# Performance work log

Measured on AMD Instinct MI355X. Metric: run time of the kernel, lower is better.

## Reference

```python
import jax, jax.numpy as jnp
from jax import lax
import numpy as np

# branch input selection (0 = real, 1 = imag) for the 8 T_att branches A..H
Q_IDX = np.array([0, 0, 1, 1, 0, 0, 1, 1])
K_IDX = np.array([0, 1, 0, 1, 0, 1, 0, 1])
V_IDX = np.array([0, 1, 1, 0, 1, 0, 0, 1])

H_DIM = 16  # LSTM hidden / out_channel


def _ln(x, w, b, eps=1e-5):
    m = x.mean(-1, keepdims=True)
    v = x.var(-1, keepdims=True)  # biased var, matches torch LayerNorm
    return (x - m) / jnp.sqrt(v + eps) * w + b


def _lstm(x, Wih, Whh, bih, bhh):
    # x: [B, T, C]; Wih: [4H, C]; Whh: [4H, H]; gate order i, f, g, o (torch)
    B = x.shape[0]
    H = Whh.shape[1]
    xg = jnp.einsum('btc,gc->btg', x, Wih) + bih + bhh  # [B, T, 4H]

    def step(carry, xg_t):
        h, c = carry
        g = xg_t + h @ Whh.T
        i, f, gg, o = jnp.split(g, 4, axis=-1)
        c = jax.nn.sigmoid(f) * c + jax.nn.sigmoid(i) * jnp.tanh(gg)
        h = jax.nn.sigmoid(o) * jnp.tanh(c)
        return (h, c), h

    h0 = jnp.zeros((B, H), x.dtype)
    _, hs = lax.scan(step, (h0, h0), jnp.swapaxes(xg, 0, 1))
    return jnp.swapaxes(hs, 0, 1)  # [B, T, H]


def _t_att(q, k, v, Wih, Whh, bih, bhh):
    # Wih: [3, 4H, C] for (query, key, value) LSTMs
    query = _lstm(q, Wih[0], Whh[0], bih[0], bhh[0])
    key = _lstm(k, Wih[1], Whh[1], bih[1], bhh[1])
    value = _lstm(v, Wih[2], Whh[2], bih[2], bhh[2])
    T = q.shape[1]
    energy = jnp.einsum('btf,bsf->bts', query, key) / 4.0  # / sqrt(16)
    mask = jnp.tril(jnp.ones((T, T), q.dtype))  # multiplicative causal mask
    energy = jax.nn.softmax(energy * mask, axis=-1)
    return jnp.einsum('bts,bsf->btf', energy, value)


def _forward(inputs, Wih, Whh, bih, bhh, ln1_w, ln1_b, ln2_w, ln2_b,
             lin_r_w, lin_r_b, lin_i_w, lin_i_b, ln3_w, ln3_b, prelu_a):
    N, C, F, T, ri = inputs.shape
    x = inputs.transpose(0, 2, 3, 1, 4).reshape(N * F, T, C, ri)  # [B, T, C, 2]
    # layernorm1 over C (applied per real/imag)
    x = jnp.swapaxes(_ln(jnp.swapaxes(x, 2, 3), ln1_w, ln1_b), 2, 3)
    real, imag = x[..., 0], x[..., 1]
    ri_stack = jnp.stack([real, imag])  # [2, B, T, C]
    q_in, k_in, v_in = ri_stack[Q_IDX], ri_stack[K_IDX], ri_stack[V_IDX]  # [8, B, T, C]
    att = jax.vmap(_t_att)(q_in, k_in, v_in, Wih, Whh, bih, bhh)  # [8, B, T, 16]
    real_att = att[0] - att[1] - att[2] - att[3]
    imag_att = att[4] + att[5] + att[6] - att[7]
    y = jnp.stack([real_att, imag_att], -1)  # [B, T, 16, 2]
    # layernorm2 over out_channel=16
    y = jnp.swapaxes(_ln(jnp.swapaxes(y, 2, 3), ln2_w, ln2_b), 2, 3)
    x_real, x_imag = y[..., 0], y[..., 1]  # [B, T, 16]
    pr = lambda z: z @ lin_r_w.T + lin_r_b
    pi = lambda z: z @ lin_i_w.T + lin_i_b
    out_real = pr(x_real) - pi(x_imag)  # [B, T, C]
    out_imag = pr(x_imag) + pi(x_real)
    out_real = out_real.reshape(N, F, T, C).transpose(0, 3, 1, 2)  # [N, C, F, T]
    out_imag = out_imag.reshape(N, F, T, C).transpose(0, 3, 1, 2)
    outs = jnp.stack([out_real, out_imag], -1)  # [N, C, F, T, 2]
    # layernorm3 over C
    outs = jnp.swapaxes(_ln(jnp.swapaxes(outs, 1, 4), ln3_w, ln3_b), 1, 4)
    outs = jnp.where(outs >= 0, outs, prelu_a * outs)  # PReLU (scalar a)
    # dropout is identity in eval mode
    return outs + inputs


def setup_inputs() -> dict:
    key = jax.random.key(0)
    ks = jax.random.split(key, 12)
    N, C, F, T = 4, 64, 100, 200
    H = H_DIM
    bound = 1.0 / np.sqrt(H)  # torch LSTM/Linear(16->64) init bound = 0.25
    u = lambda k, shape: jax.random.uniform(k, shape, jnp.float32, -bound, bound)
    return {
        'inputs': jax.random.normal(ks[0], (N, C, F, T, 2), jnp.float32),
        'Wih': u(ks[1], (8, 3, 4 * H, C)),
        'Whh': u(ks[2], (8, 3, 4 * H, H)),
        'bih': u(ks[3], (8, 3, 4 * H)),
        'bhh': u(ks[4], (8, 3, 4 * H)),
        'ln1_w': jnp.ones((C,), jnp.float32), 'ln1_b': jnp.zeros((C,), jnp.float32),
        'ln2_w': jnp.ones((H,), jnp.float32), 'ln2_b': jnp.zeros((H,), jnp.float32),
        'lin_r_w': u(ks[5], (C, H)), 'lin_r_b': u(ks[6], (C,)),
        'lin_i_w': u(ks[7], (C, H)), 'lin_i_b': u(ks[8], (C,)),
        'ln3_w': jnp.ones((C,), jnp.float32), 'ln3_b': jnp.zeros((C,), jnp.float32),
        'prelu_a': jnp.array(0.25, jnp.float32),
    }


def reference(inputs, Wih, Whh, bih, bhh, ln1_w, ln1_b, ln2_w, ln2_b,
              lin_r_w, lin_r_b, lin_i_w, lin_i_b, ln3_w, ln3_b, prelu_a):
    return _forward(inputs, Wih, Whh, bih, bhh, ln1_w, ln1_b, ln2_w, ln2_b,
                    lin_r_w, lin_r_b, lin_i_w, lin_i_b, ln3_w, ln3_b, prelu_a)
```

## Files before the change

### kernel.cpp

```cpp
#include <hip/hip_runtime.h>
#include <hip/hip_bf16.h>


typedef __attribute__((ext_vector_type(8))) short bf16x8;
typedef __attribute__((ext_vector_type(4))) float f32x4;
typedef __attribute__((ext_vector_type(2))) float f32x2;

static __device__ __forceinline__ float bf2f(unsigned short u) {
  return __uint_as_float(((unsigned)u) << 16);
}
static __device__ __forceinline__ unsigned short f2bfu(float x) {
  __hip_bfloat16 h = __float2bfloat16(x);
  return *(unsigned short*)&h;
}
static __device__ __forceinline__ float sigf(float x) {
  return __fdividef(1.f, 1.f + __expf(-x));
}
static __device__ __forceinline__ float tanh_(float x) {
  return 1.f - __fdividef(2.f, __expf(2.f * x) + 1.f);
}
static __device__ __forceinline__ f32x2 hh2(float v) {
  f32x2 r; r.x = v; r.y = v; return r;
}

template <int CTRL>
static __device__ __forceinline__ float dpp_bcast(float x) {
  int xi = __float_as_int(x);
  int r = __builtin_amdgcn_update_dpp(xi, xi, CTRL, 0xF, 0xF, false);
  return __int_as_float(r);
}

__global__ __launch_bounds__(256) void k_ln1(const float* __restrict__ in,
    const float* __restrict__ w, const float* __restrict__ bsh,
    unsigned short* __restrict__ xr, unsigned short* __restrict__ xi, int b0) {
  __shared__ float is[64][101];
  __shared__ float os[100][65];
  int bid = blockIdx.x;
  int nfl = bid >> 2, tile = bid & 3;
  int nf = b0 + nfl;
  int t0 = tile * 50;
  int n = nf / 100, f = nf - n * 100;
  int tid = threadIdx.x;
  for (int i = 0; i < 7; ++i) {
    int idx = tid + i * 256;
    if (idx < 1600) {
      int c = idx / 25, q = idx - c * 25;
      float4 v = *(const float4*)(in + (size_t)((n * 64 + c) * 100 + f) * 400
                                  + t0 * 2 + q * 4);
      is[c][q*4+0] = v.x; is[c][q*4+1] = v.y; is[c][q*4+2] = v.z; is[c][q*4+3] = v.w;
    }
  }
  __syncthreads();
  if (tid < 100) {
    float s = 0.f, ss = 0.f;
    #pragma unroll
    for (int c = 0; c < 64; ++c) { float v = is[c][tid]; s += v; ss += v * v; }
    float mean = s * 0.015625f;
    float var  = ss * 0.015625f - mean * mean;
    float rstd = rsqrtf(var + 1e-5f);
    #pragma unroll
    for (int c = 0; c < 64; ++c)
      os[tid][c] = (is[c][tid] - mean) * rstd * w[c] + bsh[c];
  }
  __syncthreads();
  for (int ri = 0; ri < 2; ++ri) {
    unsigned short* dst = ri ? xi : xr;
    for (int i = 0; i < 4; ++i) {
      int idx = tid + i * 256;
      if (idx < 800) {
        int t = idx >> 4, q = idx & 15;
        ushort4 v;
        v.x = f2bfu(os[t*2+ri][q*4+0]); v.y = f2bfu(os[t*2+ri][q*4+1]);
        v.z = f2bfu(os[t*2+ri][q*4+2]); v.w = f2bfu(os[t*2+ri][q*4+3]);
        *(ushort4*)(dst + ((size_t)nfl * 200 + t0 + t) * 64 + q * 4) = v;
      }
    }
  }
}

__global__ void k_prep(const float* __restrict__ bih, const float* __restrict__ bhh,
                       const float* __restrict__ Wih, float* __restrict__ bihh,
                       unsigned short* __restrict__ wbf) {
  int i = blockIdx.x * 256 + threadIdx.x;
  if (i < 1536) bihh[i] = bih[i] + bhh[i];
  if (i < 98304) wbf[i] = f2bfu(Wih[i]);
}

__global__ __launch_bounds__(64) void k_lstm(const unsigned short* __restrict__ xr,
    const unsigned short* __restrict__ xi, const unsigned short* __restrict__ wbf,
    const float* __restrict__ bihh, const float* __restrict__ Whh,
    float* __restrict__ hbuf, int NB, int nbq) {
  __shared__ f32x2 wl[2][16][17];
  int lane = threadIdx.x;
  int q = lane >> 4, c = lane & 15;
  int lq = blockIdx.x / nbq, q4 = blockIdx.x - lq * nbq;
  int l = lq;
  int b = q4 * 4 + q; if (b >= NB) b = NB - 1;
  const float* Wg = Whh + (size_t)l * 1024;
  for (int idx = lane; idx < 1024; idx += 64) {
    int row = idx >> 4, col = idx & 15;
    int gate = row >> 4, kk = row & 15;
    ((float*)&wl[gate >> 1][kk][col])[gate & 1] = Wg[idx];
  }
  __syncthreads();
  const f32x2* wla = wl[0][c];
  const f32x2* wlb = wl[1][c];
  int sel = (0xE54770 >> l) & 1;
  const unsigned short* xs = sel ? xi : xr;
  int ba = q4 * 4 + (c >> 2); if (ba >= NB) ba = NB - 1;
  const unsigned short* ap2 = xs + ((size_t)ba * 200 + (c & 3)) * 64 + q * 8;
  const unsigned short* wrow = wbf + l * 4096 + c * 64 + q * 8;
  float bv0 = bihh[l * 64 + c], bv1 = bihh[l * 64 + 16 + c];
  float bv2 = bihh[l * 64 + 32 + c], bv3 = bihh[l * 64 + 48 + c];
  f32x4 zb0 = {bv0, bv0, bv0, bv0}, zb1 = {bv1, bv1, bv1, bv1};
  f32x4 zb2 = {bv2, bv2, bv2, bv2}, zb3 = {bv3, bv3, bv3, bv3};
  float* hp = hbuf + ((size_t)l * NB + b) * 3200 + c;
  float h = 0.f, cs = 0.f;
  int tcur = 0;
#define MG1(DST, OFS, ZB, A0v, A1v) { \
  bf16x8 w0_ = *(const bf16x8*)(wrow + OFS); \
  bf16x8 w1_ = *(const bf16x8*)(wrow + OFS + 32); \
  f32x4 t_ = __builtin_amdgcn_mfma_f32_16x16x32_bf16(A0v, w0_, ZB, 0, 0, 0); \
  DST = __builtin_amdgcn_mfma_f32_16x16x32_bf16(A1v, w1_, t_, 0, 0, 0); }
#define MGROUP(D0, D1, D2, D3, A0v, A1v) \
  MG1(D0, 0, zb0, A0v, A1v) MG1(D1, 1024, zb1, A0v, A1v) \
  MG1(D2, 2048, zb2, A0v, A1v) MG1(D3, 3072, zb3, A0v, A1v)
#define HV(i) dpp_bcast<0x150 + i>(h)
#define LSTEP2(AC0, AC1, AC2, AC3, FLD) { \
  float hv0  = HV(0),  hv1  = HV(1),  hv2  = HV(2),  hv3  = HV(3);  \
  float hv4  = HV(4),  hv5  = HV(5),  hv6  = HV(6),  hv7  = HV(7);  \
  float hv8  = HV(8),  hv9  = HV(9),  hv10 = HV(10), hv11 = HV(11); \
  float hv12 = HV(12), hv13 = HV(13), hv14 = HV(14), hv15 = HV(15); \
  f32x2 pA = {AC0.FLD, AC1.FLD}; \
  f32x2 qA = {AC2.FLD, AC3.FLD}; \
  f32x2 pB = {0.f, 0.f}, qB = {0.f, 0.f}; \
  pA += wla[0]  * hh2(hv0);  pB += wla[1]  * hh2(hv1);  \
  qA += wlb[0]  * hh2(hv0);  qB += wlb[1]  * hh2(hv1);  \
  pA += wla[2]  * hh2(hv2);  pB += wla[3]  * hh2(hv3);  \
  qA += wlb[2]  * hh2(hv2);  qB += wlb[3]  * hh2(hv3);  \
  pA += wla[4]  * hh2(hv4);  pB += wla[5]  * hh2(hv5);  \
  qA += wlb[4]  * hh2(hv4);  qB += wlb[5]  * hh2(hv5);  \
  pA += wla[6]  * hh2(hv6);  pB += wla[7]  * hh2(hv7);  \
  qA += wlb[6]  * hh2(hv6);  qB += wlb[7]  * hh2(hv7);  \
  pA += wla[8]  * hh2(hv8);  pB += wla[9]  * hh2(hv9);  \
  qA += wlb[8]  * hh2(hv8);  qB += wlb[9]  * hh2(hv9);  \
  pA += wla[10] * hh2(hv10); pB += wla[11] * hh2(hv11); \
  qA += wlb[10] * hh2(hv10); qB += wlb[11] * hh2(hv11); \
  pA += wla[12] * hh2(hv12); pB += wla[13] * hh2(hv13); \
  qA += wlb[12] * hh2(hv12); qB += wlb[13] * hh2(hv13); \
  pA += wla[14] * hh2(hv14); pB += wla[15] * hh2(hv15); \
  qA += wlb[14] * hh2(hv14); qB += wlb[15] * hh2(hv15); \
  f32x2 p01 = pA + pB, p23 = qA + qB; \
  float ig_ = sigf(p01.x), fg_ = sigf(p01.y); \
  float gg_ = tanh_(p23.x), og_ = sigf(p23.y); \
  cs = fg_ * cs + ig_ * gg_; \
  h = og_ * tanh_(cs); \
  hp[tcur * 16] = h; ++tcur; }
  bf16x8 a0 = *(const bf16x8*)(ap2), a1 = *(const bf16x8*)(ap2 + 32);
  f32x4 c0, c1, c2, c3, n0, n1, n2, n3;
  MGROUP(c0, c1, c2, c3, a0, a1);
  ap2 += 256;
  a0 = *(const bf16x8*)(ap2); a1 = *(const bf16x8*)(ap2 + 32);
  for (int g = 0; g < 50; ++g) {
    LSTEP2(c0, c1, c2, c3, x)
    LSTEP2(c0, c1, c2, c3, y)
    MGROUP(n0, n1, n2, n3, a0, a1);
    if (g < 48) ap2 += 256;
    a0 = *(const bf16x8*)(ap2); a1 = *(const bf16x8*)(ap2 + 32);
    LSTEP2(c0, c1, c2, c3, z)
    LSTEP2(c0, c1, c2, c3, w)
    c0 = n0; c1 = n1; c2 = n2; c3 = n3;
  }
#undef LSTEP2
#undef HV
#undef MGROUP
#undef MG1
}

__global__ __launch_bounds__(256) void k_attn(const float* __restrict__ hbuf,
                                              float* __restrict__ att, int NB) {
  __shared__ float Q[200][17];
  __shared__ float K[200][16];
  __shared__ float V[200][16];
  __shared__ float Vs[200][17];
  int bid = blockIdx.x;
  int br = bid / NB, b = bid - br * NB;
  int tid = threadIdx.x;
  const float* qg = hbuf + ((size_t)(br * 3 + 0) * NB + b) * 3200;
  const float* kg = hbuf + ((size_t)(br * 3 + 1) * NB + b) * 3200;
  const float* vg = hbuf + ((size_t)(br * 3 + 2) * NB + b) * 3200;
  for (int i = 0; i < 4; ++i) {
    int idx = tid + i * 256;
    if (idx < 800) {
      int t = idx >> 2, q = idx & 3;
      float4 a = *(const float4*)(qg + t * 16 + q * 4);
      Q[t][q*4+0] = a.x; Q[t][q*4+1] = a.y; Q[t][q*4+2] = a.z; Q[t][q*4+3] = a.w;
      *(float4*)&K[t][q * 4] = *(const float4*)(kg + t * 16 + q * 4);
      *(float4*)&V[t][q * 4] = *(const float4*)(vg + t * 16 + q * 4);
    }
  }
  __syncthreads();
  if (tid < 16) {
    float acc = 0.f;
    Vs[199][tid] = 0.f;
    for (int t = 198; t >= 0; --t) { acc += V[t + 1][tid]; Vs[t][tid] = acc; }
  }
  __syncthreads();
  if (tid < 200) {
    int t = tid;
    float q0[16], va[16];
    #pragma unroll
    for (int k = 0; k < 16; ++k) q0[k] = Q[t][k] * 0.25f;
    #pragma unroll
    for (int k = 0; k < 16; ++k) va[k] = Vs[t][k];
    float S = (float)(199 - t);
    for (int s = 0; s <= t; ++s) {
      float e = 0.f;
      #pragma unroll
      for (int k = 0; k < 16; ++k) e += q0[k] * K[s][k];
      float wgt = __expf(e);
      S += wgt;
      #pragma unroll
      for (int k = 0; k < 16; ++k) va[k] += wgt * V[s][k];
    }
    float inv = __fdividef(1.f, S);
    float* dst = att + (((size_t)br * NB + b) * 200 + t) * 16;
    #pragma unroll
    for (int q = 0; q < 4; ++q) {
      float4 v; v.x = va[q*4+0]*inv; v.y = va[q*4+1]*inv;
      v.z = va[q*4+2]*inv; v.w = va[q*4+3]*inv;
      *(float4*)(dst + q * 4) = v;
    }
  }
}

__global__ __launch_bounds__(256) void k_out(const float* __restrict__ att,
    const float* __restrict__ in,
    const float* __restrict__ ln2w, const float* __restrict__ ln2b,
    const float* __restrict__ lrw, const float* __restrict__ lrb,
    const float* __restrict__ liw, const float* __restrict__ lib,
    const float* __restrict__ ln3w, const float* __restrict__ ln3b,
    const float* __restrict__ pa, float* __restrict__ out, int b0, int NB) {
  __shared__ float as_[8][40][17];
  __shared__ float ys[40][2][17];
  __shared__ float zs[64][81];
  int bid = blockIdx.x;
  int nfl = bid / 5, tile = bid - nfl * 5;
  int nf = b0 + nfl;
  int t0 = tile * 40;
  int n = nf / 100, f = nf - n * 100;
  int tid = threadIdx.x;
  for (int i = 0; i < 5; ++i) {
    int idx = tid + i * 256;
    int br = idx / 160, r = idx - br * 160;
    int t = r >> 2, q = r & 3;
    float4 v = *(const float4*)(att + (((size_t)br * NB + nfl) * 200 + t0 + t) * 16 + q * 4);
    as_[br][t][q*4+0] = v.x; as_[br][t][q*4+1] = v.y;
    as_[br][t][q*4+2] = v.z; as_[br][t][q*4+3] = v.w;
  }
  __syncthreads();
  if (tid < 80) {
    int t = tid >> 1, ri = tid & 1;
    float vv[16]; float s = 0.f, ss = 0.f;
    #pragma unroll
    for (int k = 0; k < 16; ++k) {
      float v;
      if (ri == 0) v = as_[0][t][k] - as_[1][t][k] - as_[2][t][k] - as_[3][t][k];
      else         v = as_[4][t][k] + as_[5][t][k] + as_[6][t][k] - as_[7][t][k];
      vv[k] = v; s += v; ss += v * v;
    }
    float mean = s * 0.0625f;
    float var  = ss * 0.0625f - mean * mean;
    float rstd = rsqrtf(var + 1e-5f);
    #pragma unroll
    for (int k = 0; k < 16; ++k)
      ys[t][ri][k] = (vv[k] - mean) * rstd * ln2w[k] + ln2b[k];
  }
  __syncthreads();
  int wv = tid >> 6, cc = tid & 63;
  float lr[16], li[16];
  #pragma unroll
  for (int q = 0; q < 4; ++q) {
    float4 v = *(const float4*)(lrw + cc * 16 + q * 4);
    lr[q*4+0] = v.x; lr[q*4+1] = v.y; lr[q*4+2] = v.z; lr[q*4+3] = v.w;
    float4 u = *(const float4*)(liw + cc * 16 + q * 4);
    li[q*4+0] = u.x; li[q*4+1] = u.y; li[q*4+2] = u.z; li[q*4+3] = u.w;
  }
  float brc = lrb[cc], bic = lib[cc];
  float w3 = ln3w[cc], b3 = ln3b[cc];
  float aP = pa[0];
  for (int tt = wv; tt < 40; tt += 4) {
    float zr = brc - bic, zi = brc + bic;
    #pragma unroll
    for (int k = 0; k < 16; ++k) {
      float yr = ys[tt][0][k], yi = ys[tt][1][k];
      zr += yr * lr[k] - yi * li[k];
      zi += yi * lr[k] + yr * li[k];
    }
    float s1 = zr, s2 = zr * zr, s3 = zi, s4 = zi * zi;
    #pragma unroll
    for (int m = 1; m < 64; m <<= 1) {
      s1 += __shfl_xor(s1, m, 64);
      s2 += __shfl_xor(s2, m, 64);
      s3 += __shfl_xor(s3, m, 64);
      s4 += __shfl_xor(s4, m, 64);
    }
    float mr = s1 * 0.015625f, vr = s2 * 0.015625f - mr * mr;
    float mi = s3 * 0.015625f, vi = s4 * 0.015625f - mi * mi;
    float r1 = (zr - mr) * rsqrtf(vr + 1e-5f) * w3 + b3;
    float r2 = (zi - mi) * rsqrtf(vi + 1e-5f) * w3 + b3;
    r1 = r1 >= 0.f ? r1 : aP * r1;
    r2 = r2 >= 0.f ? r2 : aP * r2;
    zs[cc][tt * 2 + 0] = r1;
    zs[cc][tt * 2 + 1] = r2;
  }
  __syncthreads();
  for (int i = 0; i < 5; ++i) {
    int idx = tid + i * 256;
    int c = idx / 20, q = idx - c * 20;
    size_t gaddr = (size_t)((n * 64 + c) * 100 + f) * 400 + t0 * 2 + q * 4;
    float4 v = *(const float4*)(in + gaddr);
    float4 z;
    z.x = zs[c][q*4+0] + v.x; z.y = zs[c][q*4+1] + v.y;
    z.z = zs[c][q*4+2] + v.z; z.w = zs[c][q*4+3] + v.w;
    *(float4*)(out + gaddr) = z;
  }
}

extern "C" void kernel_launch(void* const* d_in, const int* in_sizes, int n_in,
                              void* d_out, int out_size, void* d_ws, size_t ws_size,
                              hipStream_t stream) {
  (void)in_sizes; (void)n_in; (void)out_size;
  const float* inputs = (const float*)d_in[0];
  const float* Wih  = (const float*)d_in[1];
  const float* Whh  = (const float*)d_in[2];
  const float* bih  = (const float*)d_in[3];
  const float* bhh  = (const float*)d_in[4];
  const float* ln1w = (const float*)d_in[5];
  const float* ln1b = (const float*)d_in[6];
  const float* ln2w = (const float*)d_in[7];
  const float* ln2b = (const float*)d_in[8];
  const float* lrw  = (const float*)d_in[9];
  const float* lrb  = (const float*)d_in[10];
  const float* liw  = (const float*)d_in[11];
  const float* lib  = (const float*)d_in[12];
  const float* ln3w = (const float*)d_in[13];
  const float* ln3b = (const float*)d_in[14];
  const float* pa   = (const float*)d_in[15];
  float* out = (float*)d_out;
  char* ws = (char*)d_ws;

  int NB = 400;
  while (NB > 25 && 204800ull + (size_t)NB * 460800ull > ws_size) NB /= 2;
  int nch = 400 / NB;

  float* bihh = (float*)(ws + 0);
  unsigned short* wbf = (unsigned short*)(ws + 8192);
  size_t o_xr = 204800;
  size_t o_xi = o_xr + (size_t)NB * 25600;
  size_t o_h  = o_xi + (size_t)NB * 25600;
  size_t o_at = o_h  + (size_t)NB * 307200;
  unsigned short* xr = (unsigned short*)(ws + o_xr);
  unsigned short* xi = (unsigned short*)(ws + o_xi);
  float* hbuf = (float*)(ws + o_h);
  float* att  = (float*)(ws + o_at);

  k_prep<<<384, 256, 0, stream>>>(bih, bhh, Wih, bihh, wbf);
  int nbq = (NB + 3) >> 2;
  for (int ch = 0; ch < nch; ++ch) {
    int b0 = ch * NB;
    k_ln1 <<<NB * 4,   256, 0, stream>>>(inputs, ln1w, ln1b, xr, xi, b0);
    k_lstm<<<24 * nbq,  64, 0, stream>>>(xr, xi, wbf, bihh, Whh, hbuf, NB, nbq);
    k_attn<<<8 * NB,   256, 0, stream>>>(hbuf, att, NB);
    k_out <<<NB * 5,   256, 0, stream>>>(att, inputs, ln2w, ln2b, lrw, lrb,
                                         liw, lib, ln3w, ln3b, pa, out, b0, NB);
  }
}
```

Measured before the change: 507.8 us.

## Interleave two independent LSTM batch groups per wavefront to hide recurrence latency

Each k_lstm block now processes two groups of four sequences, interleaving their recurrent steps so the serial dpp/FMA/transcendental dependency chain of one group overlaps with the other. This halves the number of blocks and amortizes the shared-memory Whh load across more work. It raises register pressure and reduces grid size, which could lower occupancy or leave CUs idle if the block count falls below the CU count.

```diff
diff --git a/kernel.cpp b/kernel.cpp
--- a/kernel.cpp
+++ b/kernel.cpp
@@ -89,13 +89,14 @@
 __global__ __launch_bounds__(64) void k_lstm(const unsigned short* __restrict__ xr,
     const unsigned short* __restrict__ xi, const unsigned short* __restrict__ wbf,
     const float* __restrict__ bihh, const float* __restrict__ Whh,
-    float* __restrict__ hbuf, int NB, int nbq) {
+    float* __restrict__ hbuf, int NB, int nbq, int npair) {
   __shared__ f32x2 wl[2][16][17];
   int lane = threadIdx.x;
   int q = lane >> 4, c = lane & 15;
-  int lq = blockIdx.x / nbq, q4 = blockIdx.x - lq * nbq;
+  int lq = blockIdx.x / npair, pr = blockIdx.x - lq * npair;
   int l = lq;
-  int b = q4 * 4 + q; if (b >= NB) b = NB - 1;
+  int g0 = pr * 2;
+  int g1 = g0 + 1; if (g1 >= nbq) g1 = g0;
   const float* Wg = Whh + (size_t)l * 1024;
   for (int idx = lane; idx < 1024; idx += 64) {
     int row = idx >> 4, col = idx & 15;
@@ -107,16 +108,20 @@
   const f32x2* wlb = wl[1][c];
   int sel = (0xE54770 >> l) & 1;
   const unsigned short* xs = sel ? xi : xr;
-  int ba = q4 * 4 + (c >> 2); if (ba >= NB) ba = NB - 1;
-  const unsigned short* ap2 = xs + ((size_t)ba * 200 + (c & 3)) * 64 + q * 8;
+  int bA = g0 * 4 + q; if (bA >= NB) bA = NB - 1;
+  int bB = g1 * 4 + q; if (bB >= NB) bB = NB - 1;
+  int baA = g0 * 4 + (c >> 2); if (baA >= NB) baA = NB - 1;
+  int baB = g1 * 4 + (c >> 2); if (baB >= NB) baB = NB - 1;
+  const unsigned short* apA = xs + ((size_t)baA * 200 + (c & 3)) * 64 + q * 8;
+  const unsigned short* apB = xs + ((size_t)baB * 200 + (c & 3)) * 64 + q * 8;
   const unsigned short* wrow = wbf + l * 4096 + c * 64 + q * 8;
   float bv0 = bihh[l * 64 + c], bv1 = bihh[l * 64 + 16 + c];
   float bv2 = bihh[l * 64 + 32 + c], bv3 = bihh[l * 64 + 48 + c];
   f32x4 zb0 = {bv0, bv0, bv0, bv0}, zb1 = {bv1, bv1, bv1, bv1};
   f32x4 zb2 = {bv2, bv2, bv2, bv2}, zb3 = {bv3, bv3, bv3, bv3};
-  float* hp = hbuf + ((size_t)l * NB + b) * 3200 + c;
-  float h = 0.f, cs = 0.f;
-  int tcur = 0;
+  float* hpA = hbuf + ((size_t)l * NB + bA) * 3200 + c;
+  float* hpB = hbuf + ((size_t)l * NB + bB) * 3200 + c;
+  float hA = 0.f, csA = 0.f, hB = 0.f, csB = 0.f;
 #define MG1(DST, OFS, ZB, A0v, A1v) { \
   bf16x8 w0_ = *(const bf16x8*)(wrow + OFS); \
   bf16x8 w1_ = *(const bf16x8*)(wrow + OFS + 32); \
@@ -125,54 +130,66 @@
 #define MGROUP(D0, D1, D2, D3, A0v, A1v) \
   MG1(D0, 0, zb0, A0v, A1v) MG1(D1, 1024, zb1, A0v, A1v) \
   MG1(D2, 2048, zb2, A0v, A1v) MG1(D3, 3072, zb3, A0v, A1v)
-#define HV(i) dpp_bcast<0x150 + i>(h)
-#define LSTEP2(AC0, AC1, AC2, AC3, FLD) { \
-  float hv0  = HV(0),  hv1  = HV(1),  hv2  = HV(2),  hv3  = HV(3);  \
-  float hv4  = HV(4),  hv5  = HV(5),  hv6  = HV(6),  hv7  = HV(7);  \
-  float hv8  = HV(8),  hv9  = HV(9),  hv10 = HV(10), hv11 = HV(11); \
-  float hv12 = HV(12), hv13 = HV(13), hv14 = HV(14), hv15 = HV(15); \
-  f32x2 pA = {AC0.FLD, AC1.FLD}; \
-  f32x2 qA = {AC2.FLD, AC3.FLD}; \
-  f32x2 pB = {0.f, 0.f}, qB = {0.f, 0.f}; \
-  pA += wla[0]  * hh2(hv0);  pB += wla[1]  * hh2(hv1);  \
-  qA += wlb[0]  * hh2(hv0);  qB += wlb[1]  * hh2(hv1);  \
-  pA += wla[2]  * hh2(hv2);  pB += wla[3]  * hh2(hv3);  \
-  qA += wlb[2]  * hh2(hv2);  qB += wlb[3]  * hh2(hv3);  \
-  pA += wla[4]  * hh2(hv4);  pB += wla[5]  * hh2(hv5);  \
-  qA += wlb[4]  * hh2(hv4);  qB += wlb[5]  * hh2(hv5);  \
-  pA += wla[6]  * hh2(hv6);  pB += wla[7]  * hh2(hv7);  \
-  qA += wlb[6]  * hh2(hv6);  qB += wlb[7]  * hh2(hv7);  \
-  pA += wla[8]  * hh2(hv8);  pB += wla[9]  * hh2(hv9);  \
-  qA += wlb[8]  * hh2(hv8);  qB += wlb[9]  * hh2(hv9);  \
-  pA += wla[10] * hh2(hv10); pB += wla[11] * hh2(hv11); \
-  qA += wlb[10] * hh2(hv10); qB += wlb[11] * hh2(hv11); \
-  pA += wla[12] * hh2(hv12); pB += wla[13] * hh2(hv13); \
-  qA += wlb[12] * hh2(hv12); qB += wlb[13] * hh2(hv13); \
-  pA += wla[14] * hh2(hv14); pB += wla[15] * hh2(hv15); \
-  qA += wlb[14] * hh2(hv14); qB += wlb[15] * hh2(hv15); \
-  f32x2 p01 = pA + pB, p23 = qA + qB; \
+#define HVX(i, H) dpp_bcast<0x150 + i>(H)
+#define LSTEP2(H, CS, HP, AC0, AC1, AC2, AC3, FLD, TT) { \
+  float hv0  = HVX(0,H),  hv1  = HVX(1,H),  hv2  = HVX(2,H),  hv3  = HVX(3,H);  \
+  float hv4  = HVX(4,H),  hv5  = HVX(5,H),  hv6  = HVX(6,H),  hv7  = HVX(7,H);  \
+  float hv8  = HVX(8,H),  hv9  = HVX(9,H),  hv10 = HVX(10,H), hv11 = HVX(11,H); \
+  float hv12 = HVX(12,H), hv13 = HVX(13,H), hv14 = HVX(14,H), hv15 = HVX(15,H); \
+  f32x2 pA_ = {AC0.FLD, AC1.FLD}; \
+  f32x2 qA_ = {AC2.FLD, AC3.FLD}; \
+  f32x2 pB_ = {0.f, 0.f}, qB_ = {0.f, 0.f}; \
+  pA_ += wla[0]  * hh2(hv0);  pB_ += wla[1]  * hh2(hv1);  \
+  qA_ += wlb[0]  * hh2(hv0);  qB_ += wlb[1]  * hh2(hv1);  \
+  pA_ += wla[2]  * hh2(hv2);  pB_ += wla[3]  * hh2(hv3);  \
+  qA_ += wlb[2]  * hh2(hv2);  qB_ += wlb[3]  * hh2(hv3);  \
+  pA_ += wla[4]  * hh2(hv4);  pB_ += wla[5]  * hh2(hv5);  \
+  qA_ += wlb[4]  * hh2(hv4);  qB_ += wlb[5]  * hh2(hv5);  \
+  pA_ += wla[6]  * hh2(hv6);  pB_ += wla[7]  * hh2(hv7);  \
+  qA_ += wlb[6]  * hh2(hv6);  qB_ += wlb[7]  * hh2(hv7);  \
+  pA_ += wla[8]  * hh2(hv8);  pB_ += wla[9]  * hh2(hv9);  \
+  qA_ += wlb[8]  * hh2(hv8);  qB_ += wlb[9]  * hh2(hv9);  \
+  pA_ += wla[10] * hh2(hv10); pB_ += wla[11] * hh2(hv11); \
+  qA_ += wlb[10] * hh2(hv10); qB_ += wlb[11] * hh2(hv11); \
+  pA_ += wla[12] * hh2(hv12); pB_ += wla[13] * hh2(hv13); \
+  qA_ += wlb[12] * hh2(hv12); qB_ += wlb[13] * hh2(hv13); \
+  pA_ += wla[14] * hh2(hv14); pB_ += wla[15] * hh2(hv15); \
+  qA_ += wlb[14] * hh2(hv14); qB_ += wlb[15] * hh2(hv15); \
+  f32x2 p01 = pA_ + pB_, p23 = qA_ + qB_; \
   float ig_ = sigf(p01.x), fg_ = sigf(p01.y); \
   float gg_ = tanh_(p23.x), og_ = sigf(p23.y); \
-  cs = fg_ * cs + ig_ * gg_; \
-  h = og_ * tanh_(cs); \
-  hp[tcur * 16] = h; ++tcur; }
-  bf16x8 a0 = *(const bf16x8*)(ap2), a1 = *(const bf16x8*)(ap2 + 32);
-  f32x4 c0, c1, c2, c3, n0, n1, n2, n3;
-  MGROUP(c0, c1, c2, c3, a0, a1);
-  ap2 += 256;
-  a0 = *(const bf16x8*)(ap2); a1 = *(const bf16x8*)(ap2 + 32);
+  CS = fg_ * CS + ig_ * gg_; \
+  H = og_ * tanh_(CS); \
+  HP[(TT) * 16] = H; }
+  bf16x8 aA0 = *(const bf16x8*)(apA), aA1 = *(const bf16x8*)(apA + 32);
+  bf16x8 aB0 = *(const bf16x8*)(apB), aB1 = *(const bf16x8*)(apB + 32);
+  f32x4 cA0, cA1, cA2, cA3, nA0, nA1, nA2, nA3;
+  f32x4 cB0, cB1, cB2, cB3, nB0, nB1, nB2, nB3;
+  MGROUP(cA0, cA1, cA2, cA3, aA0, aA1);
+  MGROUP(cB0, cB1, cB2, cB3, aB0, aB1);
+  apA += 256; apB += 256;
+  aA0 = *(const bf16x8*)(apA); aA1 = *(const bf16x8*)(apA + 32);
+  aB0 = *(const bf16x8*)(apB); aB1 = *(const bf16x8*)(apB + 32);
   for (int g = 0; g < 50; ++g) {
-    LSTEP2(c0, c1, c2, c3, x)
-    LSTEP2(c0, c1, c2, c3, y)
-    MGROUP(n0, n1, n2, n3, a0, a1);
-    if (g < 48) ap2 += 256;
-    a0 = *(const bf16x8*)(ap2); a1 = *(const bf16x8*)(ap2 + 32);
-    LSTEP2(c0, c1, c2, c3, z)
-    LSTEP2(c0, c1, c2, c3, w)
-    c0 = n0; c1 = n1; c2 = n2; c3 = n3;
+    int t4 = g * 4;
+    LSTEP2(hA, csA, hpA, cA0, cA1, cA2, cA3, x, t4)
+    LSTEP2(hB, csB, hpB, cB0, cB1, cB2, cB3, x, t4)
+    LSTEP2(hA, csA, hpA, cA0, cA1, cA2, cA3, y, t4 + 1)
+    LSTEP2(hB, csB, hpB, cB0, cB1, cB2, cB3, y, t4 + 1)
+    MGROUP(nA0, nA1, nA2, nA3, aA0, aA1);
+    MGROUP(nB0, nB1, nB2, nB3, aB0, aB1);
+    if (g < 48) { apA += 256; apB += 256; }
+    aA0 = *(const bf16x8*)(apA); aA1 = *(const bf16x8*)(apA + 32);
+    aB0 = *(const bf16x8*)(apB); aB1 = *(const bf16x8*)(apB + 32);
+    LSTEP2(hA, csA, hpA, cA0, cA1, cA2, cA3, z, t4 + 2)
+    LSTEP2(hB, csB, hpB, cB0, cB1, cB2, cB3, z, t4 + 2)
+    LSTEP2(hA, csA, hpA, cA0, cA1, cA2, cA3, w, t4 + 3)
+    LSTEP2(hB, csB, hpB, cB0, cB1, cB2, cB3, w, t4 + 3)
+    cA0 = nA0; cA1 = nA1; cA2 = nA2; cA3 = nA3;
+    cB0 = nB0; cB1 = nB1; cB2 = nB2; cB3 = nB3;
   }
 #undef LSTEP2
-#undef HV
+#undef HVX
 #undef MGROUP
 #undef MG1
 }
@@ -367,12 +384,14 @@
 
   k_prep<<<384, 256, 0, stream>>>(bih, bhh, Wih, bihh, wbf);
   int nbq = (NB + 3) >> 2;
+  int npair = (nbq + 1) >> 1;
   for (int ch = 0; ch < nch; ++ch) {
     int b0 = ch * NB;
-    k_ln1 <<<NB * 4,   256, 0, stream>>>(inputs, ln1w, ln1b, xr, xi, b0);
-    k_lstm<<<24 * nbq,  64, 0, stream>>>(xr, xi, wbf, bihh, Whh, hbuf, NB, nbq);
-    k_attn<<<8 * NB,   256, 0, stream>>>(hbuf, att, NB);
-    k_out <<<NB * 5,   256, 0, stream>>>(att, inputs, ln2w, ln2b, lrw, lrb,
-                                         liw, lib, ln3w, ln3b, pa, out, b0, NB);
-  }
-}
+    k_ln1 <<<NB * 4,     256, 0, stream>>>(inputs, ln1w, ln1b, xr, xi, b0);
+    k_lstm<<<24 * npair,  64, 0, stream>>>(xr, xi, wbf, bihh, Whh, hbuf,
+                                           NB, nbq, npair);
+    k_attn<<<8 * NB,     256, 0, stream>>>(hbuf, att, NB);
+    k_out <<<NB * 5,     256, 0, stream>>>(att, inputs, ln2w, ln2b, lrw, lrb,
+                                           liw, lib, ln3w, ln3b, pa, out, b0, NB);
+  }
+}
```

Result: slower. 566.5 us (+11.6%).

## Compute causal attention with bf16 MFMA tiles for QK and PV

Applied to the files above, without the earlier changes.

Replaces the scalar per-row attention loop with wave-level 16x16x32 bf16 MFMA tiles. Each wave computes QK scores, exponentiates them with the multiplicative-mask semantics (masked keys get weight 1), and stages P in LDS to feed a second MFMA against V stored transposed. Row sums are reduced with shuffles. The intent is to cut the serial per-thread dot-product cost. In exchange, Q, K, V and P are rounded to bf16, and the kernel reads padded rows past t=199.

```diff
diff --git a/kernel.cpp b/kernel.cpp
--- a/kernel.cpp
+++ b/kernel.cpp
@@ -179,58 +179,91 @@
 
 __global__ __launch_bounds__(256) void k_attn(const float* __restrict__ hbuf,
                                               float* __restrict__ att, int NB) {
-  __shared__ float Q[200][17];
-  __shared__ float K[200][16];
-  __shared__ float V[200][16];
-  __shared__ float Vs[200][17];
+  __shared__ unsigned short Kb[224][40];
+  __shared__ unsigned short Vt[16][232];
+  __shared__ unsigned short Pc[4][16][40];
   int bid = blockIdx.x;
   int br = bid / NB, b = bid - br * NB;
   int tid = threadIdx.x;
   const float* qg = hbuf + ((size_t)(br * 3 + 0) * NB + b) * 3200;
   const float* kg = hbuf + ((size_t)(br * 3 + 1) * NB + b) * 3200;
   const float* vg = hbuf + ((size_t)(br * 3 + 2) * NB + b) * 3200;
+  {
+    unsigned* kz = (unsigned*)&Kb[0][0];
+    for (int i = tid; i < 4480; i += 256) kz[i] = 0;
+    unsigned* vz = (unsigned*)&Vt[0][0];
+    for (int i = tid; i < 1856; i += 256) vz[i] = 0;
+  }
+  __syncthreads();
   for (int i = 0; i < 4; ++i) {
     int idx = tid + i * 256;
     if (idx < 800) {
-      int t = idx >> 2, q = idx & 3;
-      float4 a = *(const float4*)(qg + t * 16 + q * 4);
-      Q[t][q*4+0] = a.x; Q[t][q*4+1] = a.y; Q[t][q*4+2] = a.z; Q[t][q*4+3] = a.w;
-      *(float4*)&K[t][q * 4] = *(const float4*)(kg + t * 16 + q * 4);
-      *(float4*)&V[t][q * 4] = *(const float4*)(vg + t * 16 + q * 4);
-    }
-  }
-  __syncthreads();
-  if (tid < 16) {
-    float acc = 0.f;
-    Vs[199][tid] = 0.f;
-    for (int t = 198; t >= 0; --t) { acc += V[t + 1][tid]; Vs[t][tid] = acc; }
-  }
-  __syncthreads();
-  if (tid < 200) {
-    int t = tid;
-    float q0[16], va[16];
-    #pragma unroll
-    for (int k = 0; k < 16; ++k) q0[k] = Q[t][k] * 0.25f;
-    #pragma unroll
-    for (int k = 0; k < 16; ++k) va[k] = Vs[t][k];
-    float S = (float)(199 - t);
-    for (int s = 0; s <= t; ++s) {
-      float e = 0.f;
+      int s = idx >> 2, qq = idx & 3;
+      float4 kv = *(const float4*)(kg + s * 16 + qq * 4);
+      ushort4 kp;
+      kp.x = f2bfu(kv.x); kp.y = f2bfu(kv.y);
+      kp.z = f2bfu(kv.z); kp.w = f2bfu(kv.w);
+      *(ushort4*)&Kb[s][qq * 4] = kp;
+      float4 vv = *(const float4*)(vg + s * 16 + qq * 4);
+      Vt[qq * 4 + 0][s] = f2bfu(vv.x);
+      Vt[qq * 4 + 1][s] = f2bfu(vv.y);
+      Vt[qq * 4 + 2][s] = f2bfu(vv.z);
+      Vt[qq * 4 + 3][s] = f2bfu(vv.w);
+    }
+  }
+  __syncthreads();
+  int w = tid >> 6, lane = tid & 63;
+  int q = lane >> 4, n = lane & 15;
+  size_t obase = (size_t)(br * NB + b) * 200;
+  for (int m = w; m <= 12; m += 4) {
+    bf16x8 aQ;
+    {
+      int trow = 16 * m + n;
+      const float* qp = qg + trow * 16 + q * 8;
       #pragma unroll
-      for (int k = 0; k < 16; ++k) e += q0[k] * K[s][k];
-      float wgt = __expf(e);
-      S += wgt;
+      for (int e = 0; e < 8; ++e) {
+        float v = (q < 2) ? qp[e] * 0.25f : 0.f;
+        aQ[e] = (short)f2bfu(v);
+      }
+    }
+    f32x4 pv = {0.f, 0.f, 0.f, 0.f};
+    float s40 = 0.f, s41 = 0.f, s42 = 0.f, s43 = 0.f;
+    #pragma unroll 1
+    for (int jj = 0; jj < 7; ++jj) {
+      int sb = jj * 32;
+      bf16x8 bK0 = *(const bf16x8*)&Kb[sb + n][q * 8];
+      bf16x8 bK1 = *(const bf16x8*)&Kb[sb + 16 + n][q * 8];
+      f32x4 z = {0.f, 0.f, 0.f, 0.f};
+      f32x4 d0 = __builtin_amdgcn_mfma_f32_16x16x32_bf16(aQ, bK0, z, 0, 0, 0);
+      f32x4 d1 = __builtin_amdgcn_mfma_f32_16x16x32_bf16(aQ, bK1, z, 0, 0, 0);
+      int s0 = sb + n, s1 = sb + 16 + n;
+      int tb = 16 * m + 4 * q;
       #pragma unroll
-      for (int k = 0; k < 16; ++k) va[k] += wgt * V[s][k];
-    }
-    float inv = __fdividef(1.f, S);
-    float* dst = att + (((size_t)br * NB + b) * 200 + t) * 16;
-    #pragma unroll
-    for (int q = 0; q < 4; ++q) {
-      float4 v; v.x = va[q*4+0]*inv; v.y = va[q*4+1]*inv;
-      v.z = va[q*4+2]*inv; v.w = va[q*4+3]*inv;
-      *(float4*)(dst + q * 4) = v;
-    }
+      for (int r = 0; r < 4; ++r) {
+        int t = tb + r;
+        float p0 = (s0 > 199) ? 0.f : ((s0 > t) ? 1.f : __expf(d0[r]));
+        float p1 = (s1 > 199) ? 0.f : ((s1 > t) ? 1.f : __expf(d1[r]));
+        if (r == 0) { s40 += p0 + p1; } else if (r == 1) { s41 += p0 + p1; }
+        else if (r == 2) { s42 += p0 + p1; } else { s43 += p0 + p1; }
+        Pc[w][4 * q + r][n]      = f2bfu(p0);
+        Pc[w][4 * q + r][16 + n] = f2bfu(p1);
+      }
+      bf16x8 aP = *(const bf16x8*)&Pc[w][n][q * 8];
+      bf16x8 bV = *(const bf16x8*)&Vt[n][sb + q * 8];
+      pv = __builtin_amdgcn_mfma_f32_16x16x32_bf16(aP, bV, pv, 0, 0, 0);
+    }
+    #pragma unroll
+    for (int mm = 1; mm < 16; mm <<= 1) {
+      s40 += __shfl_xor(s40, mm, 64);
+      s41 += __shfl_xor(s41, mm, 64);
+      s42 += __shfl_xor(s42, mm, 64);
+      s43 += __shfl_xor(s43, mm, 64);
+    }
+    int tb = 16 * m + 4 * q;
+    if (tb + 0 < 200) att[(obase + tb + 0) * 16 + n] = pv[0] * __fdividef(1.f, s40);
+    if (tb + 1 < 200) att[(obase + tb + 1) * 16 + n] = pv[1] * __fdividef(1.f, s41);
+    if (tb + 2 < 200) att[(obase + tb + 2) * 16 + n] = pv[2] * __fdividef(1.f, s42);
+    if (tb + 3 < 200) att[(obase + tb + 3) * 16 + n] = pv[3] * __fdividef(1.f, s43);
   }
 }
 
```

Result: faster. 420.7 us (-17.1%).
